# Optimization experiments

Hardware: AMD Instinct MI355X
Metric: run time of the kernel (lower is better)

The kernel has to match this reference:

```python
import jax, jax.numpy as jnp
import numpy as np

DIST = 7
ROUNDS = 25
A = DIST ** 2 - 1              # n_ancillas = 48
ND = A * (A + 1) // 2          # 1176 upper-triangular entries


def _triangular_polmap():
    diag, nondiag = [], []
    for iy in range(A):
        for ix in range(iy, A):
            if ix != iy:
                nondiag.append(ix + iy * A)
            else:
                diag.append(ix + iy * A)
    return np.asarray(diag + nondiag, dtype=np.int32)

POLMAP = jnp.asarray(_triangular_polmap())  # (ND,)


def setup_inputs() -> dict:
    key = jax.random.key(0)
    k1, k2, k3 = jax.random.split(key, 3)
    x = jax.random.randint(k1, (4096, ROUNDS, A), 0, 2, dtype=jnp.int32)
    emb_diag = jax.random.normal(k2, (1, A), dtype=jnp.float32)
    emb_nondiag = jax.random.normal(k3, (1, ND - A, 4), dtype=jnp.float32)
    return {"x": x, "emb_diag": emb_diag, "emb_nondiag": emb_nondiag}


def reference(x, emb_diag, emb_nondiag):
    B, R, _ = x.shape
    # transformed embedding params (shared across rounds / batch via broadcast)
    sig_diag = jax.nn.sigmoid(emb_diag)                       # (1, A)
    f12 = jax.nn.sigmoid(emb_nondiag[:, :, 0])
    f9 = jax.nn.sigmoid(emb_nondiag[:, :, 1]) * f12
    f8 = jax.nn.sigmoid(emb_nondiag[:, :, 2]) * f9
    f6 = jax.nn.sigmoid(emb_nondiag[:, :, 3]) * f8
    fnd = jnp.stack([f12, f9, f8, f6], axis=2)                # (1, ND-A, 4)

    # sliding windows of 3 consecutive rounds, round axis leading for scan
    a = jnp.moveaxis(x[:, 0:R - 2, :], 1, 0)                  # (R-2, B, A)
    b = jnp.moveaxis(x[:, 1:R - 1, :], 1, 0)
    c = jnp.moveaxis(x[:, 2:R, :], 1, 0)

    def step(carry, abc):
        st, dt = carry                                         # int32 (B, A)
        ai, bi, ci = abc
        data_err = ai + ci - ai * ci * 2
        meas_err = bi * (1 - (ai + ci)) + ai * ci
        dt = dt * (1 - meas_err * 2)
        st = jnp.clip(st + dt * data_err, -1, 1)
        dt = dt * (1 - st * st * (1 - meas_err)) - st * (1 - meas_err)
        # quadratic (outer-product) state, values in {4,6,8,9,12,16}
        xx = st + 3
        outer = (xx[:, :, None] * xx[:, None, :]).reshape(B, A * A)
        tri = jnp.take(outer, POLMAP, axis=1)                  # (B, ND)
        rd, rn = tri[:, :A], tri[:, A:]
        diag_val = (rd == 16).astype(jnp.float32) + (rd == 9).astype(jnp.float32) * sig_diag
        nmask = jnp.stack([rn == 12, rn == 9, rn == 8, rn == 6], axis=2).astype(jnp.float32)
        nd_val = (rn == 16).astype(jnp.float32) + jnp.sum(nmask * fnd, axis=2)
        out = jnp.concatenate([diag_val, nd_val], axis=1)      # (B, ND)
        return (st, dt), out

    st0 = -jnp.ones((B, A), jnp.int32)
    dt0 = jnp.ones((B, A), jnp.int32)
    _, ys = jax.lax.scan(step, (st0, dt0), (a, b, c))          # (R-2, B, ND)
    return jnp.moveaxis(ys, 0, 1)                              # (B, R-2, ND)
```

## Files before the change

### kernel.cpp

```cpp
#include <hip/hip_runtime.h>
#include <math.h>

#define AA 48
#define RR 25
#define TT 23
#define ND 1176
#define NOFF 1128
#define BPB 4
#define NTHREADS 256

__global__ __launch_bounds__(NTHREADS) void cnn_embed_kernel(
    const int*   __restrict__ x,
    const float* __restrict__ emb_diag,
    const float* __restrict__ emb_nd,
    float*       __restrict__ out,
    int B)
{
    __shared__ uint8_t  xls[BPB * RR * AA];
    __shared__ uint8_t  xxc[BPB * TT * AA];
    __shared__ uint16_t pairs[ND];
    __shared__ float4   gtab[ND];

    const int tid = threadIdx.x;
    const int b0  = blockIdx.x * BPB;

    for (int p = tid; p < AA; p += NTHREADS) {
        pairs[p] = (uint16_t)(p | (p << 8));
        float s = 1.0f / (1.0f + __expf(-emb_diag[p]));
        gtab[p] = make_float4(0.0f, s, 0.0f, 0.0f);
    }
    for (int pp = tid; pp < NOFF; pp += NTHREADS) {
        int iy = (int)((95.0f - sqrtf(9025.0f - 8.0f * (float)pp)) * 0.5f);
        if (iy < 0) iy = 0;
        if (iy > 46) iy = 46;
        while (iy < 46 && (47 * (iy + 1) - ((iy + 1) * iy) / 2) <= pp) ++iy;
        while (iy > 0 && (47 * iy - (iy * (iy - 1)) / 2) > pp) --iy;
        int S  = 47 * iy - (iy * (iy - 1)) / 2;
        int ix = iy + 1 + (pp - S);
        pairs[AA + pp] = (uint16_t)(iy | (ix << 8));
        const float* e = emb_nd + pp * 4;
        float f12 = 1.0f / (1.0f + __expf(-e[0]));
        float f9  = f12 / (1.0f + __expf(-e[1]));
        float f8  = f9  / (1.0f + __expf(-e[2]));
        float f6  = f8  / (1.0f + __expf(-e[3]));
        gtab[AA + pp] = make_float4(f12, f9, f8, f6);
    }

    {
        int validB = B - b0;
        if (validB > BPB) validB = BPB;
        const int validInts = validB * RR * AA;
        const int4* xg = (const int4*)(x + (size_t)b0 * RR * AA);
        for (int g = tid; g * 4 < validInts; g += NTHREADS) {
            int4 v = xg[g];
            uint32_t packed = (uint32_t)(v.x & 1) | ((uint32_t)(v.y & 1) << 8) |
                              ((uint32_t)(v.z & 1) << 16) | ((uint32_t)(v.w & 1) << 24);
            *((uint32_t*)&xls[g * 4]) = packed;
        }
    }
    __syncthreads();

    if (tid < BPB * AA) {
        const int bb = tid / AA;
        const int j  = tid - bb * AA;
        if (b0 + bb < B) {
            const uint8_t* xb  = &xls[bb * RR * AA];
            uint8_t*       xxb = &xxc[bb * TT * AA];
            int st = -1, dt = 1;
            for (int t = 0; t < TT; ++t) {
                int a  = xb[t * AA + j];
                int bv = xb[(t + 1) * AA + j];
                int c  = xb[(t + 2) * AA + j];
                int de = a ^ c;
                int me = de ? 0 : (a ^ bv);
                if (me) dt = -dt;
                st += dt * de;
                st = st < -1 ? -1 : (st > 1 ? 1 : st);
                if (!me) dt = (st == 0) ? dt : -st;
                xxb[t * AA + j] = (uint8_t)(st + 3);
            }
        }
    }
    __syncthreads();

    for (int bb = 0; bb < BPB; ++bb) {
        const int b = b0 + bb;
        if (b >= B) break;
        const uint8_t* xxb = &xxc[bb * TT * AA];
        float* ob = out + (size_t)b * TT * ND;
        for (int t = 0; t < TT; ++t) {
            const uint8_t* xr = &xxb[t * AA];
            float* orow = ob + t * ND;
            for (int p = tid; p < ND; p += NTHREADS) {
                uint32_t pr = pairs[p];
                int i  = pr & 0xFF;
                int jj = pr >> 8;
                int prod = (int)xr[i] * (int)xr[jj];
                float4 g = gtab[p];
                float v = 0.0f;
                v = (prod == 6)  ? g.w : v;
                v = (prod == 8)  ? g.z : v;
                v = (prod == 9)  ? g.y : v;
                v = (prod == 12) ? g.x : v;
                v = (prod == 16) ? 1.0f : v;
                orow[p] = v;
            }
        }
    }
}

extern "C" void kernel_launch(void* const* d_in, const int* in_sizes, int n_in,
                              void* d_out, int out_size, void* d_ws, size_t ws_size,
                              hipStream_t stream) {
    const int*   x  = (const int*)d_in[0];
    const float* ed = (const float*)d_in[1];
    const float* en = (const float*)d_in[2];
    float* out = (float*)d_out;
    const int B = in_sizes[0] / (RR * AA);
    const int grid = (B + BPB - 1) / BPB;
    hipLaunchKernelGGL(cnn_embed_kernel, dim3(grid), dim3(NTHREADS), 0, stream,
                       x, ed, en, out, B);
}
```

Measured before the change: 528.3 us.

## Precompute embedding tables in a separate kernel and store float4 per thread

Moves the sigmoid table and pair-index construction out of every block into a small prologue kernel that writes to workspace. Each main-kernel thread then holds 4 consecutive output columns' indices and gains in registers (294 owners, 320 threads) and writes float4-vectorised rows. This removes the per-block transcendental and sqrt setup work and the shared-memory table, and turns scalar stores into 16-byte stores. The cost is a second launch, higher register pressure and a few idle threads.

```diff
diff --git a/kernel.cpp b/kernel.cpp
--- a/kernel.cpp
+++ b/kernel.cpp
@@ -7,29 +7,25 @@
 #define ND 1176
 #define NOFF 1128
 #define BPB 4
-#define NTHREADS 256
+#define NT 320
+#define NOWN 294
 
-__global__ __launch_bounds__(NTHREADS) void cnn_embed_kernel(
-    const int*   __restrict__ x,
+#define GTAB_BYTES (ND * 16)
+
+__global__ __launch_bounds__(256) void build_tables_kernel(
     const float* __restrict__ emb_diag,
     const float* __restrict__ emb_nd,
-    float*       __restrict__ out,
-    int B)
+    float4* __restrict__ gtab,
+    uint32_t* __restrict__ pairs)
 {
-    __shared__ uint8_t  xls[BPB * RR * AA];
-    __shared__ uint8_t  xxc[BPB * TT * AA];
-    __shared__ uint16_t pairs[ND];
-    __shared__ float4   gtab[ND];
-
-    const int tid = threadIdx.x;
-    const int b0  = blockIdx.x * BPB;
-
-    for (int p = tid; p < AA; p += NTHREADS) {
-        pairs[p] = (uint16_t)(p | (p << 8));
+    int p = blockIdx.x * 256 + threadIdx.x;
+    if (p >= ND) return;
+    if (p < AA) {
+        pairs[p] = (uint32_t)(p | (p << 8));
         float s = 1.0f / (1.0f + __expf(-emb_diag[p]));
         gtab[p] = make_float4(0.0f, s, 0.0f, 0.0f);
-    }
-    for (int pp = tid; pp < NOFF; pp += NTHREADS) {
+    } else {
+        int pp = p - AA;
         int iy = (int)((95.0f - sqrtf(9025.0f - 8.0f * (float)pp)) * 0.5f);
         if (iy < 0) iy = 0;
         if (iy > 46) iy = 46;
@@ -37,13 +33,40 @@
         while (iy > 0 && (47 * iy - (iy * (iy - 1)) / 2) > pp) --iy;
         int S  = 47 * iy - (iy * (iy - 1)) / 2;
         int ix = iy + 1 + (pp - S);
-        pairs[AA + pp] = (uint16_t)(iy | (ix << 8));
+        pairs[p] = (uint32_t)(iy | (ix << 8));
         const float* e = emb_nd + pp * 4;
         float f12 = 1.0f / (1.0f + __expf(-e[0]));
         float f9  = f12 / (1.0f + __expf(-e[1]));
         float f8  = f9  / (1.0f + __expf(-e[2]));
         float f6  = f8  / (1.0f + __expf(-e[3]));
-        gtab[AA + pp] = make_float4(f12, f9, f8, f6);
+        gtab[p] = make_float4(f12, f9, f8, f6);
+    }
+}
+
+__global__ __launch_bounds__(NT) void cnn_embed_kernel(
+    const int*      __restrict__ x,
+    const float4*   __restrict__ gtab,
+    const uint32_t* __restrict__ pairs,
+    float*          __restrict__ out,
+    int B)
+{
+    __shared__ uint8_t xls[BPB * RR * AA];
+    __shared__ uint8_t xxc[BPB * TT * AA];
+
+    const int tid = threadIdx.x;
+    const int b0  = blockIdx.x * BPB;
+
+    const bool owner = (tid < NOWN);
+    int iidx[4], jidx[4];
+    float4 g[4];
+    if (owner) {
+        uint4 pr = ((const uint4*)pairs)[tid];
+        iidx[0] = pr.x & 0xFF; jidx[0] = (pr.x >> 8) & 0xFF;
+        iidx[1] = pr.y & 0xFF; jidx[1] = (pr.y >> 8) & 0xFF;
+        iidx[2] = pr.z & 0xFF; jidx[2] = (pr.z >> 8) & 0xFF;
+        iidx[3] = pr.w & 0xFF; jidx[3] = (pr.w >> 8) & 0xFF;
+        #pragma unroll
+        for (int k = 0; k < 4; ++k) g[k] = gtab[4 * tid + k];
     }
 
     {
@@ -51,11 +74,11 @@
         if (validB > BPB) validB = BPB;
         const int validInts = validB * RR * AA;
         const int4* xg = (const int4*)(x + (size_t)b0 * RR * AA);
-        for (int g = tid; g * 4 < validInts; g += NTHREADS) {
-            int4 v = xg[g];
+        for (int gg = tid; gg * 4 < validInts; gg += NT) {
+            int4 v = xg[gg];
             uint32_t packed = (uint32_t)(v.x & 1) | ((uint32_t)(v.y & 1) << 8) |
                               ((uint32_t)(v.z & 1) << 16) | ((uint32_t)(v.w & 1) << 24);
-            *((uint32_t*)&xls[g * 4]) = packed;
+            *((uint32_t*)&xls[gg * 4]) = packed;
         }
     }
     __syncthreads();
@@ -67,6 +90,7 @@
             const uint8_t* xb  = &xls[bb * RR * AA];
             uint8_t*       xxb = &xxc[bb * TT * AA];
             int st = -1, dt = 1;
+            #pragma unroll
             for (int t = 0; t < TT; ++t) {
                 int a  = xb[t * AA + j];
                 int bv = xb[(t + 1) * AA + j];
@@ -83,27 +107,29 @@
     }
     __syncthreads();
 
-    for (int bb = 0; bb < BPB; ++bb) {
-        const int b = b0 + bb;
-        if (b >= B) break;
-        const uint8_t* xxb = &xxc[bb * TT * AA];
-        float* ob = out + (size_t)b * TT * ND;
-        for (int t = 0; t < TT; ++t) {
-            const uint8_t* xr = &xxb[t * AA];
-            float* orow = ob + t * ND;
-            for (int p = tid; p < ND; p += NTHREADS) {
-                uint32_t pr = pairs[p];
-                int i  = pr & 0xFF;
-                int jj = pr >> 8;
-                int prod = (int)xr[i] * (int)xr[jj];
-                float4 g = gtab[p];
-                float v = 0.0f;
-                v = (prod == 6)  ? g.w : v;
-                v = (prod == 8)  ? g.z : v;
-                v = (prod == 9)  ? g.y : v;
-                v = (prod == 12) ? g.x : v;
-                v = (prod == 16) ? 1.0f : v;
-                orow[p] = v;
+    if (owner) {
+        #pragma unroll
+        for (int bb = 0; bb < BPB; ++bb) {
+            const int b = b0 + bb;
+            if (b >= B) break;
+            const uint8_t* xxb = &xxc[bb * TT * AA];
+            float* ob = out + (size_t)b * TT * ND + tid * 4;
+            for (int t = 0; t < TT; ++t) {
+                const uint8_t* xr = &xxb[t * AA];
+                float4 v;
+                float* vf = (float*)&v;
+                #pragma unroll
+                for (int k = 0; k < 4; ++k) {
+                    int prod = (int)xr[iidx[k]] * (int)xr[jidx[k]];
+                    float r = 0.0f;
+                    r = (prod == 6)  ? g[k].w : r;
+                    r = (prod == 8)  ? g[k].z : r;
+                    r = (prod == 9)  ? g[k].y : r;
+                    r = (prod == 12) ? g[k].x : r;
+                    r = (prod == 16) ? 1.0f   : r;
+                    vf[k] = r;
+                }
+                *((float4*)(ob + t * ND)) = v;
             }
         }
     }
@@ -116,8 +142,13 @@
     const float* ed = (const float*)d_in[1];
     const float* en = (const float*)d_in[2];
     float* out = (float*)d_out;
+    float4*   gtab  = (float4*)d_ws;
+    uint32_t* pairs = (uint32_t*)((char*)d_ws + GTAB_BYTES);
     const int B = in_sizes[0] / (RR * AA);
+
+    hipLaunchKernelGGL(build_tables_kernel, dim3((ND + 255) / 256), dim3(256), 0, stream,
+                       ed, en, gtab, pairs);
     const int grid = (B + BPB - 1) / BPB;
-    hipLaunchKernelGGL(cnn_embed_kernel, dim3(grid), dim3(NTHREADS), 0, stream,
-                       x, ed, en, out, B);
+    hipLaunchKernelGGL(cnn_embed_kernel, dim3(grid), dim3(NT), 0, stream,
+                       x, gtab, pairs, out, B);
 }
```

After: 483.7 us. -8.4%, faster.
